# Optimization experiments

Hardware: AMD Instinct MI355X
Metric: run time of the kernel (lower is better)

## Reference

```python
import math
import jax, jax.numpy as jnp
import numpy as np

B, C, NH, H, W = 8, 512, 4, 64, 64
CH = C // 8          # qkv channels = 64
HC = CH // NH        # head channels = 16


def _pos_encoding(c, h, w):
    # Faithful to torch code, including the raw memory reinterpretation of
    # pos_h (h, c) -> (1, c, h, 1) and pos_w (c//2, 2w) -> (1, c, 1, w).
    ph = jnp.arange(h, dtype=jnp.float32)[:, None]            # (h, 1)
    pw = jnp.arange(w, dtype=jnp.float32)[None, :]            # (1, w)
    div = jnp.exp(jnp.arange(0, c, 2, dtype=jnp.float32) * (-(math.log(10000.0) / c)))
    pos_h = ph * div[None, :]                                  # (h, c/2)
    pos_w = pw * div[:, None]                                  # (c/2, w)
    pos_h = jnp.concatenate([jnp.sin(pos_h), jnp.cos(pos_h)], axis=1)  # (h, c)
    pos_w = jnp.concatenate([jnp.sin(pos_w), jnp.cos(pos_w)], axis=1)  # (c/2, 2w)
    pos_h = pos_h.reshape(1, c, h, 1)   # raw view, as in torch
    pos_w = pos_w.reshape(1, c, 1, w)   # raw view, as in torch
    return pos_h + pos_w                # (1, c, h, w)


def _conv1x1(x, w, b):
    return jnp.einsum('bchw,oc->bohw', x, w) + b[None, :, None, None]


def setup_inputs() -> dict:
    key = jax.random.key(0)
    ks = jax.random.split(key, 6)
    s = 0.02
    return {
        'x':  jax.random.normal(ks[0], (B, C, H, W), dtype=jnp.float32),
        'wq': jax.random.normal(ks[1], (CH, C), dtype=jnp.float32) * s,
        'bq': jnp.zeros((CH,), dtype=jnp.float32),
        'wk': jax.random.normal(ks[2], (CH, C), dtype=jnp.float32) * s,
        'bk': jnp.zeros((CH,), dtype=jnp.float32),
        'wv': jax.random.normal(ks[3], (CH, C), dtype=jnp.float32) * s,
        'bv': jnp.zeros((CH,), dtype=jnp.float32),
        'wo': jax.random.normal(ks[4], (C, CH), dtype=jnp.float32) * s,
        'bo': jnp.zeros((C,), dtype=jnp.float32),
        'gamma': jnp.full((1,), 0.5, dtype=jnp.float32),  # nonzero to exercise whole graph
    }


def reference(x, wq, bq, wk, bk, wv, bv, wo, bo, gamma):
    b, c, h, w = x.shape
    nh, hc = NH, HC
    x = x + _pos_encoding(c, h, w)

    q = _conv1x1(x, wq, bq).reshape(b, nh, hc, h, w)
    k = _conv1x1(x, wk, bk).reshape(b, nh, hc, h, w)
    v = _conv1x1(x, wv, bv).reshape(b, nh, hc, h, w)

    # column (H) and row (W) views
    q_H = q.transpose(0, 1, 4, 2, 3).reshape(b * nh * w, hc, h).transpose(0, 2, 1)  # (bnw, h, hc)
    q_W = q.transpose(0, 1, 3, 2, 4).reshape(b * nh * h, hc, w).transpose(0, 2, 1)  # (bnh, w, hc)
    k_H = k.transpose(0, 1, 4, 2, 3).reshape(b * nh * w, hc, h)
    k_W = k.transpose(0, 1, 3, 2, 4).reshape(b * nh * h, hc, w)
    v_H = v.transpose(0, 1, 4, 2, 3).reshape(b * nh * w, hc, h)
    v_W = v.transpose(0, 1, 3, 2, 4).reshape(b * nh * h, hc, w)

    inf_mask = jnp.where(jnp.eye(h, dtype=bool), -jnp.inf, 0.0).astype(x.dtype)  # (h, h)
    energy_H = (jnp.matmul(q_H, k_H) + inf_mask[None]).reshape(b, nh, w, h, h).transpose(0, 2, 1, 3, 4)  # (b,w,nh,h,h)
    energy_W = jnp.matmul(q_W, k_W).reshape(b, nh, h, w, w).transpose(0, 2, 1, 3, 4)                     # (b,h,nh,w,w)

    conc = jax.nn.softmax(jnp.concatenate([energy_H, energy_W], axis=4), axis=4)  # (b,w,nh,h,h+w)

    att_H = conc[..., :h].transpose(0, 2, 1, 3, 4).reshape(b * nh * w, h, h)
    # NOTE: faithful to torch: (b,h,nh,w,w) is flattened in (b,h,nh) order
    att_W = conc[..., h:h + w].reshape(b * nh * h, w, w)

    out_H = jnp.matmul(v_H, att_H.transpose(0, 2, 1))
    out_H = out_H.reshape(b, nh, w, hc, h).transpose(0, 3, 4, 1, 2).reshape(b, nh * hc, h, w)
    out_W = jnp.matmul(v_W, att_W.transpose(0, 2, 1))
    out_W = out_W.reshape(b, nh, h, hc, w).transpose(0, 3, 1, 4, 2).reshape(b, nh * hc, h, w)

    out = _conv1x1(out_H + out_W, wo, bo)
    return gamma * out + x
```

## Files before the change

kernel.cpp:

```cpp
#include <hip/hip_runtime.h>
#include <math.h>


typedef unsigned int u32;
typedef unsigned short u16;
typedef __attribute__((ext_vector_type(8))) short short8;
typedef __attribute__((ext_vector_type(4))) float f32x4;

__device__ __forceinline__ u16 f2bf(float v) {
    u32 u = __float_as_uint(v);
    u32 r = (u + 0x7FFFu + ((u >> 16) & 1u)) >> 16;
    return (u16)r;
}

__device__ __forceinline__ float bf2f(u16 v) {
    return __uint_as_float(((u32)v) << 16);
}

__device__ __forceinline__ void gll16(const void* g, void* l) {
    __builtin_amdgcn_global_load_lds(
        (const __attribute__((address_space(1))) u32*)g,
        (__attribute__((address_space(3))) u32*)l, 16, 0, 0);
}

__global__ __launch_bounds__(64) void pos_kernel(float* __restrict__ PH,
                                                 float* __restrict__ PW) {
    const float r = 0.03597789207798663f;
    int c = blockIdx.x;
    int t = threadIdx.x;
    int i = c >> 3;
    int j = ((c & 7) << 6) | t;
    float ph;
    if (j < 256) ph = sinf((float)i * expf(-(float)j * r));
    else         ph = cosf((float)i * expf(-(float)(j - 256) * r));
    PH[c * 64 + t] = ph;
    int tt = c >> 1;
    float dv = expf(-(float)tt * r);
    PW[c * 64 + t] = (c & 1) ? cosf((float)t * dv) : sinf((float)t * dv);
}

__global__ __launch_bounds__(256) void wconv_kernel(
    const float* __restrict__ wq, const float* __restrict__ wk,
    const float* __restrict__ wv, const float* __restrict__ wo,
    u16* __restrict__ WT, u16* __restrict__ WOb) {
    int i = blockIdx.x * 256 + threadIdx.x;
    if (i < 98304) {
        float v;
        if (i < 32768)      v = wq[i];
        else if (i < 65536) v = wk[i - 32768];
        else                v = wv[i - 65536];
        WT[i] = f2bf(v);
    } else {
        WOb[i - 98304] = f2bf(wo[i - 98304]);
    }
}

__global__ __launch_bounds__(256) void xpose_kernel(
    const float* __restrict__ x, const float* __restrict__ PH,
    const float* __restrict__ PW, u16* __restrict__ XT) {
    __shared__ u16 T[64 * 68];
    int ct = blockIdx.x;
    int pt = blockIdx.y;
    int b  = blockIdx.z;
    int tid = threadIdx.x;
    int c0 = ct * 64;
    const size_t xb = ((size_t)b * 512 + c0) * 4096 + pt * 64;
#pragma unroll
    for (int it = 0; it < 16; ++it) {
        int idx = tid + it * 256;
        int cl = idx >> 6, pl = idx & 63;
        float v = x[xb + (size_t)cl * 4096 + pl]
                + PH[(c0 + cl) * 64 + pt] + PW[(c0 + cl) * 64 + pl];
        T[pl * 68 + cl] = f2bf(v);
    }
    __syncthreads();
#pragma unroll
    for (int jt = 0; jt < 4; ++jt) {
        int row = jt * 16 + (tid >> 4);
        int cq  = tid & 15;
        ushort4 val = *(const ushort4*)&T[row * 68 + cq * 4];
        *(ushort4*)&XT[((size_t)b * 4096 + pt * 64 + row) * 512 + c0 + cq * 4] = val;
    }
}

__global__ __launch_bounds__(256) void qkvm_kernel(
    const u16* __restrict__ XT, const u16* __restrict__ WT,
    const float* __restrict__ bq, const float* __restrict__ bk,
    const float* __restrict__ bv,
    u16* __restrict__ QHt, u16* __restrict__ QWt,
    u16* __restrict__ KHt, u16* __restrict__ KWt,
    u16* __restrict__ VHt, u16* __restrict__ Vb) {
    __shared__ u16 Ab[64 * 64];
    __shared__ u16 Bb[128 * 64];
    int pt = blockIdx.x;
    int mg = blockIdx.y;
    int b  = blockIdx.z;
    int tid  = threadIdx.x;
    int w    = tid >> 6;
    int lane = tid & 63;
    int ln15 = lane & 15, quad = lane >> 4;
    int p0 = pt * 128;
    const u16* Wg = WT + mg * 64 * 512;
    const u16* Xg = XT + ((size_t)b * 4096 + p0) * 512;

    f32x4 acc[4][2];
#pragma unroll
    for (int mf = 0; mf < 4; ++mf)
#pragma unroll
        for (int pf = 0; pf < 2; ++pf)
            acc[mf][pf] = (f32x4){0.f, 0.f, 0.f, 0.f};

    for (int kc = 0; kc < 512; kc += 64) {
        __syncthreads();
#pragma unroll
        for (int it = 0; it < 2; ++it) {
            int idx = tid + it * 256;
            int r = idx >> 3, s = idx & 7;
            gll16(Wg + r * 512 + kc + ((s ^ (r & 7)) * 8), &Ab[idx * 8]);
        }
#pragma unroll
        for (int it = 0; it < 4; ++it) {
            int idx = tid + it * 256;
            int r = idx >> 3, s = idx & 7;
            gll16(Xg + (size_t)r * 512 + kc + ((s ^ (r & 7)) * 8), &Bb[idx * 8]);
        }
        __syncthreads();
#pragma unroll
        for (int ks = 0; ks < 2; ++ks) {
            int cs = ks * 4 + quad;
            short8 af[4], bf[2];
#pragma unroll
            for (int mf = 0; mf < 4; ++mf) {
                int row = mf * 16 + ln15;
                af[mf] = *(const short8*)&Ab[row * 64 + ((cs ^ (row & 7)) * 8)];
            }
#pragma unroll
            for (int pf = 0; pf < 2; ++pf) {
                int row = w * 32 + pf * 16 + ln15;
                bf[pf] = *(const short8*)&Bb[row * 64 + ((cs ^ (row & 7)) * 8)];
            }
#pragma unroll
            for (int mf = 0; mf < 4; ++mf)
#pragma unroll
                for (int pf = 0; pf < 2; ++pf)
                    acc[mf][pf] = __builtin_amdgcn_mfma_f32_16x16x32_bf16(
                        af[mf], bf[pf], acc[mf][pf], 0, 0, 0);
        }
    }

    const float* bias = (mg == 0) ? bq : (mg == 1) ? bk : bv;
    if (mg == 2) {
#pragma unroll
        for (int mf = 0; mf < 4; ++mf)
#pragma unroll
            for (int pf = 0; pf < 2; ++pf) {
                int p = p0 + w * 32 + pf * 16 + ln15;
                int h = p >> 6, wc = p & 63;
#pragma unroll
                for (int reg = 0; reg < 4; ++reg) {
                    int hc = quad * 4 + reg;
                    int m  = mf * 16 + hc;
                    u16 bfv = f2bf(acc[mf][pf][reg] + bias[m]);
                    VHt[(((b * 4 + mf) * 64 + wc) * 16 + hc) * 64 + h] = bfv;
                    Vb[((size_t)(b * 64 + m)) * 4096 + p] = bfv;
                }
            }
    } else {
        u16* Ht = (mg == 1) ? KHt : QHt;
        u16* Wt = (mg == 1) ? KWt : QWt;
#pragma unroll
        for (int mf = 0; mf < 4; ++mf)
#pragma unroll
            for (int pf = 0; pf < 2; ++pf) {
                int p = p0 + w * 32 + pf * 16 + ln15;
                int h = p >> 6, wc = p & 63;
                ushort4 pk;
                pk.x = f2bf(acc[mf][pf][0] + bias[mf * 16 + quad * 4 + 0]);
                pk.y = f2bf(acc[mf][pf][1] + bias[mf * 16 + quad * 4 + 1]);
                pk.z = f2bf(acc[mf][pf][2] + bias[mf * 16 + quad * 4 + 2]);
                pk.w = f2bf(acc[mf][pf][3] + bias[mf * 16 + quad * 4 + 3]);
                *(ushort4*)&Ht[(((b * 4 + mf) * 64 + wc) * 64 + h) * 16 + quad * 4] = pk;
                *(ushort4*)&Wt[(((b * 4 + mf) * 64 + h) * 64 + wc) * 16 + quad * 4] = pk;
            }
    }
}

__global__ __launch_bounds__(256, 4) void attn_kernel(
    const u16* __restrict__ QHt, const u16* __restrict__ QWt,
    const u16* __restrict__ KHt, const u16* __restrict__ KWt,
    const u16* __restrict__ VHt, const u16* __restrict__ Vb,
    u16* __restrict__ OHc, u16* __restrict__ OWc) {
    __shared__ u16 A_lds[64 * 40];
    __shared__ u16 B_lds[128 * 40];
    __shared__ u16 VH_lds[16 * 72];
    __shared__ u16 VW_lds[16 * 72];
    __shared__ u16 P_lds[64 * 152];

    int a = blockIdx.x, n = blockIdx.y, b = blockIdx.z;
    int tid  = threadIdx.x;
    int w    = tid >> 6;
    int lane = tid & 63;
    int ln15 = lane & 15, quad = lane >> 4;
    int nv = a >> 4;
    int hv = ((a & 15) << 2) | n;

    const int cb = ((b * 4 + n) * 64 + a) << 10;
    const u16* vb = Vb + ((size_t)(b * 64 + nv * 16)) * 4096 + hv * 64;

    {
        int t = tid & 127;
        const short8 z8 = {0, 0, 0, 0, 0, 0, 0, 0};
        if (tid < 128) {
            short8 vA = *(const short8*)(QHt + cb + t * 8);
            *(short8*)&A_lds[(t >> 1) * 40 + (t & 1) * 8] = vA;
            short8 vK = *(const short8*)(KHt + cb + t * 8);
            *(short8*)&B_lds[(t >> 1) * 40 + (t & 1) * 8] = vK;
            *(short8*)&B_lds[(t >> 1) * 40 + 16 + (t & 1) * 8] = z8;
            short8 vV = *(const short8*)(VHt + cb + t * 8);
            *(short8*)&VH_lds[(t >> 3) * 72 + (t & 7) * 8] = vV;
        } else {
            short8 vA = *(const short8*)(QWt + cb + t * 8);
            *(short8*)&A_lds[(t >> 1) * 40 + 16 + (t & 1) * 8] = vA;
            short8 vK = *(const short8*)(KWt + cb + t * 8);
            *(short8*)&B_lds[(64 + (t >> 1)) * 40 + 16 + (t & 1) * 8] = vK;
            *(short8*)&B_lds[(64 + (t >> 1)) * 40 + (t & 1) * 8] = z8;
            short8 vV = *(const short8*)(vb + (t >> 3) * 4096 + (t & 7) * 8);
            *(short8*)&VW_lds[(t >> 3) * 72 + (t & 7) * 8] = vV;
        }
    }
    __syncthreads();

    const f32x4 zf = {0.f, 0.f, 0.f, 0.f};
    short8 af = *(const short8*)&A_lds[(w * 16 + ln15) * 40 + quad * 8];
    f32x4 acc[8];
#pragma unroll
    for (int nt = 0; nt < 8; ++nt) {
        short8 bf = *(const short8*)&B_lds[(nt * 16 + ln15) * 40 + quad * 8];
        acc[nt] = __builtin_amdgcn_mfma_f32_16x16x32_bf16(af, bf, zf, 0, 0, 0);
    }

#pragma unroll
    for (int nt = 0; nt < 4; ++nt)
#pragma unroll
        for (int r = 0; r < 4; ++r)
            if (nt * 16 + ln15 == w * 16 + quad * 4 + r) acc[nt][r] = -1e30f;

    float inv[4];
#pragma unroll
    for (int r = 0; r < 4; ++r) {
        float mrow = acc[0][r];
#pragma unroll
        for (int nt = 1; nt < 8; ++nt) mrow = fmaxf(mrow, acc[nt][r]);
        mrow = fmaxf(mrow, __shfl_xor(mrow, 1, 64));
        mrow = fmaxf(mrow, __shfl_xor(mrow, 2, 64));
        mrow = fmaxf(mrow, __shfl_xor(mrow, 4, 64));
        mrow = fmaxf(mrow, __shfl_xor(mrow, 8, 64));
        float s = 0.f;
#pragma unroll
        for (int nt = 0; nt < 8; ++nt) {
            float e = __expf(acc[nt][r] - mrow);
            acc[nt][r] = e;
            s += e;
        }
        s += __shfl_xor(s, 1, 64);
        s += __shfl_xor(s, 2, 64);
        s += __shfl_xor(s, 4, 64);
        s += __shfl_xor(s, 8, 64);
        inv[r] = 1.0f / s;
    }
#pragma unroll
    for (int nt = 0; nt < 8; ++nt)
#pragma unroll
        for (int r = 0; r < 4; ++r)
            P_lds[(w * 16 + quad * 4 + r) * 152 + nt * 16 + ln15] =
                f2bf(acc[nt][r] * inv[r]);
    __syncthreads();

    int prow = (w * 16 + ln15) * 152;
    short8 a0 = *(const short8*)&P_lds[prow +       quad * 8];
    short8 a1 = *(const short8*)&P_lds[prow + 32  + quad * 8];
    short8 a2 = *(const short8*)&P_lds[prow + 64  + quad * 8];
    short8 a3 = *(const short8*)&P_lds[prow + 96  + quad * 8];
    short8 b0 = *(const short8*)&VH_lds[ln15 * 72 +      quad * 8];
    short8 b1 = *(const short8*)&VH_lds[ln15 * 72 + 32 + quad * 8];
    short8 c0 = *(const short8*)&VW_lds[ln15 * 72 +      quad * 8];
    short8 c1 = *(const short8*)&VW_lds[ln15 * 72 + 32 + quad * 8];
    f32x4 oH = __builtin_amdgcn_mfma_f32_16x16x32_bf16(a0, b0, zf, 0, 0, 0);
    oH = __builtin_amdgcn_mfma_f32_16x16x32_bf16(a1, b1, oH, 0, 0, 0);
    f32x4 oW = __builtin_amdgcn_mfma_f32_16x16x32_bf16(a2, c0, zf, 0, 0, 0);
    oW = __builtin_amdgcn_mfma_f32_16x16x32_bf16(a3, c1, oW, 0, 0, 0);

    __syncthreads();
    u16* eph = P_lds;
    u16* epw = P_lds + 16 * 68;
#pragma unroll
    for (int r = 0; r < 4; ++r) {
        eph[(quad * 4 + r) * 68 + ln15 * 4 + w]   = f2bf(oH[r]);
        epw[(w * 16 + quad * 4 + r) * 20 + ln15]  = f2bf(oW[r]);
    }
    __syncthreads();
    {
        int t = tid;
        ushort4 vh = *(const ushort4*)&eph[(t >> 4) * 68 + (t & 15) * 4];
        ushort4 vw = *(const ushort4*)&epw[(t >> 2) * 20 + (t & 3) * 4];
        size_t cbase = (((size_t)b * 4 + n) * 64 + a) * 1024;
        *(ushort4*)&OHc[cbase + t * 4] = vh;
        *(ushort4*)&OWc[cbase + t * 4] = vw;
    }
}

__global__ __launch_bounds__(256) void sconv_kernel(
    const u16* __restrict__ OHc, const u16* __restrict__ OWc,
    u16* __restrict__ Sb) {
    int h = blockIdx.x;
    int b = blockIdx.y;
    int t  = threadIdx.x;
    int wp = t >> 2;
    int cq = t & 3;

    const u16* ohp = OHc + ((((size_t)b * 4 + (h & 3)) * 64 + wp) * 1024
                            + (h >> 2) * 64 + cq * 16);
    short8 oh0 = *(const short8*)ohp;
    short8 oh1 = *(const short8*)(ohp + 8);

    const u16* owb = OWc + (((size_t)b * 4 + (wp & 3)) * 64) * 1024 + h * 16 + cq * 4;
    ushort4 owv[4];
#pragma unroll
    for (int nvi = 0; nvi < 4; ++nvi)
        owv[nvi] = *(const ushort4*)(owb + (size_t)((nvi << 4) | (wp >> 2)) * 1024);

    u16 res[16];
#pragma unroll
    for (int j = 0; j < 16; ++j) {
        u16 ohv = (j < 8) ? (u16)oh0[j] : (u16)oh1[j - 8];
        const ushort4& q = owv[j & 3];
        u16 owu = (j >> 2) == 0 ? q.x : (j >> 2) == 1 ? q.y : (j >> 2) == 2 ? q.z : q.w;
        res[j] = f2bf(bf2f(ohv) + bf2f(owu));
    }
    u16* dst = Sb + (((size_t)b * 4096 + h * 64 + wp) * 64 + cq * 16);
    *(short8*)dst       = *(short8*)&res[0];
    *(short8*)(dst + 8) = *(short8*)&res[8];
}

__global__ __launch_bounds__(256, 4) void finalm_kernel(
    const u16* __restrict__ Sb, const u16* __restrict__ WOb,
    const float* __restrict__ bo, const float* __restrict__ gamma,
    const float* __restrict__ x, const float* __restrict__ PH,
    const float* __restrict__ PW, float* __restrict__ out) {
    __shared__ u16 Ab[64 * 64];
    __shared__ u16 Bb[128 * 64];
    int pt = blockIdx.x;
    int mc = blockIdx.y;
    int b  = blockIdx.z;
    int tid  = threadIdx.x;
    int w    = tid >> 6;
    int lane = tid & 63;
    int ln15 = lane & 15, quad = lane >> 4;
    int p0 = pt * 128, m0 = mc * 64;

    float4 xv[4][2];
#pragma unroll
    for (int mf = 0; mf < 4; ++mf) {
        int m = m0 + mf * 16 + ln15;
#pragma unroll
        for (int pf = 0; pf < 2; ++pf) {
            int pb = p0 + w * 32 + pf * 16 + quad * 4;
            xv[mf][pf] = *(const float4*)&x[((size_t)(b * 512 + m)) * 4096 + pb];
        }
    }

    const u16* Ag = WOb + m0 * 64;
    const u16* Sg = Sb + ((size_t)b * 4096 + p0) * 64;

#pragma unroll
    for (int it = 0; it < 2; ++it) {
        int idx = tid + it * 256;
        int r = idx >> 3, s = idx & 7;
        gll16(Ag + r * 64 + ((s ^ (r & 7)) * 8), &Ab[idx * 8]);
    }
#pragma unroll
    for (int it = 0; it < 4; ++it) {
        int idx = tid + it * 256;
        int r = idx >> 3, s = idx & 7;
        gll16(Sg + r * 64 + ((s ^ (r & 7)) * 8), &Bb[idx * 8]);
    }
    __syncthreads();

    const f32x4 zf = {0.f, 0.f, 0.f, 0.f};
    f32x4 acc[4][2];
#pragma unroll
    for (int mf = 0; mf < 4; ++mf)
#pragma unroll
        for (int pf = 0; pf < 2; ++pf)
            acc[mf][pf] = zf;
#pragma unroll
    for (int ks = 0; ks < 2; ++ks) {
        int cs = ks * 4 + quad;
        short8 af[2], bf[4];
#pragma unroll
        for (int pf = 0; pf < 2; ++pf) {
            int row = w * 32 + pf * 16 + ln15;
            af[pf] = *(const short8*)&Bb[row * 64 + ((cs ^ (row & 7)) * 8)];
        }
#pragma unroll
        for (int mf = 0; mf < 4; ++mf) {
            int row = mf * 16 + ln15;
            bf[mf] = *(const short8*)&Ab[row * 64 + ((cs ^ (row & 7)) * 8)];
        }
#pragma unroll
        for (int mf = 0; mf < 4; ++mf)
#pragma unroll
            for (int pf = 0; pf < 2; ++pf)
                acc[mf][pf] = __builtin_amdgcn_mfma_f32_16x16x32_bf16(
                    af[pf], bf[mf], acc[mf][pf], 0, 0, 0);
    }

    float g = gamma[0];
    int h = pt * 2 + (w >> 1);
    int plb = (w & 1) * 32;
#pragma unroll
    for (int mf = 0; mf < 4; ++mf) {
        int m = m0 + mf * 16 + ln15;
        float bm = bo[m];
        float ph = PH[m * 64 + h];
#pragma unroll
        for (int pf = 0; pf < 2; ++pf) {
            int pb = p0 + w * 32 + pf * 16 + quad * 4;
            size_t o = ((size_t)(b * 512 + m)) * 4096 + pb;
            float4 pwv = *(const float4*)&PW[m * 64 + plb + pf * 16 + quad * 4];
            float4 res;
            res.x = g * (acc[mf][pf][0] + bm) + xv[mf][pf].x + ph + pwv.x;
            res.y = g * (acc[mf][pf][1] + bm) + xv[mf][pf].y + ph + pwv.y;
            res.z = g * (acc[mf][pf][2] + bm) + xv[mf][pf].z + ph + pwv.z;
            res.w = g * (acc[mf][pf][3] + bm) + xv[mf][pf].w + ph + pwv.w;
            *(float4*)&out[o] = res;
        }
    }
}

extern "C" void kernel_launch(void* const* d_in, const int* in_sizes, int n_in,
                              void* d_out, int out_size, void* d_ws, size_t ws_size,
                              hipStream_t stream) {
    const float* x     = (const float*)d_in[0];
    const float* wq    = (const float*)d_in[1];
    const float* bq    = (const float*)d_in[2];
    const float* wk    = (const float*)d_in[3];
    const float* bk    = (const float*)d_in[4];
    const float* wv    = (const float*)d_in[5];
    const float* bv    = (const float*)d_in[6];
    const float* wo    = (const float*)d_in[7];
    const float* bo    = (const float*)d_in[8];
    const float* gamma = (const float*)d_in[9];
    float* out = (float*)d_out;
    float* ws  = (float*)d_ws;

    float* PH = ws;
    float* PW = PH + 32768;
    u16*   WT  = (u16*)(PW + 32768);
    u16*   WOb = WT + 98304;
    u16*   XT  = WOb + 32768;
    u16*   QHt = XT + 16777216;
    u16*   QWt = QHt + 2097152;
    u16*   KHt = QWt + 2097152;
    u16*   KWt = KHt + 2097152;
    u16*   VHt = KWt + 2097152;
    u16*   Vb  = VHt + 2097152;
    u16*   OHc = XT;
    u16*   OWc = OHc + 2097152;
    u16*   Sbb = OWc + 2097152;

    pos_kernel<<<dim3(512), dim3(64), 0, stream>>>(PH, PW);
    wconv_kernel<<<dim3(512), dim3(256), 0, stream>>>(wq, wk, wv, wo, WT, WOb);
    xpose_kernel<<<dim3(8, 64, 8), dim3(256), 0, stream>>>(x, PH, PW, XT);
    qkvm_kernel<<<dim3(32, 3, 8), dim3(256), 0, stream>>>(
        XT, WT, bq, bk, bv, QHt, QWt, KHt, KWt, VHt, Vb);
    attn_kernel<<<dim3(64, 4, 8), dim3(256), 0, stream>>>(
        QHt, QWt, KHt, KWt, VHt, Vb, OHc, OWc);
    sconv_kernel<<<dim3(64, 8), dim3(256), 0, stream>>>(OHc, OWc, Sbb);
    finalm_kernel<<<dim3(32, 8, 8), dim3(256), 0, stream>>>(
        Sbb, WOb, bo, gamma, x, PH, PW, out);
}
```

Measured before the change: 207.7 us.

## Fuse x transpose into QKV GEMM and fold positional encoding into weight projections

Removes the separate transpose kernel that wrote a bf16 copy of x plus positional encoding. The QKV kernel now reads fp32 x directly, converts it to bf16 in LDS, and computes all 192 output channels per block, so each x tile is loaded once. The positional-encoding contribution is precomputed as W·PH and W·PW tables by a small kernel and added in the epilogue, using linearity of the 1x1 conv. The attention kernel also packs its LDS buffers into one shared union with smaller strides to raise occupancy, which needs an extra barrier before P is written. The risks are uncoalesced-ish strided x loads and the positional term being added in fp32 rather than quantised with x.

```diff
diff --git a/kernel.cpp b/kernel.cpp
--- a/kernel.cpp
+++ b/kernel.cpp
@@ -55,133 +55,117 @@
     }
 }
 
-__global__ __launch_bounds__(256) void xpose_kernel(
-    const float* __restrict__ x, const float* __restrict__ PH,
-    const float* __restrict__ PW, u16* __restrict__ XT) {
-    __shared__ u16 T[64 * 68];
-    int ct = blockIdx.x;
-    int pt = blockIdx.y;
-    int b  = blockIdx.z;
-    int tid = threadIdx.x;
-    int c0 = ct * 64;
-    const size_t xb = ((size_t)b * 512 + c0) * 4096 + pt * 64;
-#pragma unroll
-    for (int it = 0; it < 16; ++it) {
-        int idx = tid + it * 256;
-        int cl = idx >> 6, pl = idx & 63;
-        float v = x[xb + (size_t)cl * 4096 + pl]
-                + PH[(c0 + cl) * 64 + pt] + PW[(c0 + cl) * 64 + pl];
-        T[pl * 68 + cl] = f2bf(v);
-    }
-    __syncthreads();
-#pragma unroll
-    for (int jt = 0; jt < 4; ++jt) {
-        int row = jt * 16 + (tid >> 4);
-        int cq  = tid & 15;
-        ushort4 val = *(const ushort4*)&T[row * 68 + cq * 4];
-        *(ushort4*)&XT[((size_t)b * 4096 + pt * 64 + row) * 512 + c0 + cq * 4] = val;
-    }
-}
-
-__global__ __launch_bounds__(256) void qkvm_kernel(
-    const u16* __restrict__ XT, const u16* __restrict__ WT,
+__global__ __launch_bounds__(256) void wpos_kernel(
+    const float* __restrict__ wq, const float* __restrict__ wk,
+    const float* __restrict__ wv,
+    const float* __restrict__ PH, const float* __restrict__ PW,
+    float* __restrict__ WPH3, float* __restrict__ WPW3) {
+    int gid = blockIdx.x * 256 + threadIdx.x;
+    int h = gid & 63;
+    int m = (gid >> 6) & 63;
+    int t = gid >> 12;
+    int mg = t >> 1, tbl = t & 1;
+    const float* W = (mg == 0) ? wq : (mg == 1) ? wk : wv;
+    const float* P = tbl ? PW : PH;
+    const float* wr = W + m * 512;
+    float s = 0.f;
+#pragma unroll 8
+    for (int c = 0; c < 512; ++c) s += wr[c] * P[c * 64 + h];
+    (tbl ? WPW3 : WPH3)[(mg * 64 + m) * 64 + h] = s;
+}
+
+__global__ __launch_bounds__(256) void qkvx_kernel(
+    const float* __restrict__ x, const u16* __restrict__ WT,
     const float* __restrict__ bq, const float* __restrict__ bk,
     const float* __restrict__ bv,
+    const float* __restrict__ WPH3, const float* __restrict__ WPW3,
     u16* __restrict__ QHt, u16* __restrict__ QWt,
     u16* __restrict__ KHt, u16* __restrict__ KWt,
     u16* __restrict__ VHt, u16* __restrict__ Vb) {
-    __shared__ u16 Ab[64 * 64];
-    __shared__ u16 Bb[128 * 64];
-    int pt = blockIdx.x;
-    int mg = blockIdx.y;
-    int b  = blockIdx.z;
+    __shared__ u16 Wb[192 * 64];
+    __shared__ u16 Bb[64 * 64];
+    int L  = blockIdx.x;
+    int b  = L & 7;
+    int pt = L >> 3;
     int tid  = threadIdx.x;
     int w    = tid >> 6;
     int lane = tid & 63;
     int ln15 = lane & 15, quad = lane >> 4;
-    int p0 = pt * 128;
-    const u16* Wg = WT + mg * 64 * 512;
-    const u16* Xg = XT + ((size_t)b * 4096 + p0) * 512;
-
-    f32x4 acc[4][2];
-#pragma unroll
-    for (int mf = 0; mf < 4; ++mf)
-#pragma unroll
-        for (int pf = 0; pf < 2; ++pf)
-            acc[mf][pf] = (f32x4){0.f, 0.f, 0.f, 0.f};
+
+    f32x4 acc[12];
+#pragma unroll
+    for (int mf = 0; mf < 12; ++mf) acc[mf] = (f32x4){0.f, 0.f, 0.f, 0.f};
+
+    const float* xb = x + (size_t)b * 2097152 + pt * 64;
 
     for (int kc = 0; kc < 512; kc += 64) {
         __syncthreads();
 #pragma unroll
-        for (int it = 0; it < 2; ++it) {
+        for (int it = 0; it < 6; ++it) {
             int idx = tid + it * 256;
             int r = idx >> 3, s = idx & 7;
-            gll16(Wg + r * 512 + kc + ((s ^ (r & 7)) * 8), &Ab[idx * 8]);
-        }
-#pragma unroll
-        for (int it = 0; it < 4; ++it) {
-            int idx = tid + it * 256;
-            int r = idx >> 3, s = idx & 7;
-            gll16(Xg + (size_t)r * 512 + kc + ((s ^ (r & 7)) * 8), &Bb[idx * 8]);
+            gll16(WT + r * 512 + kc + ((s ^ (r & 7)) * 8), &Wb[idx * 8]);
+        }
+#pragma unroll
+        for (int j = 0; j < 2; ++j) {
+            int cc = w + j * 4;
+            const float* xp = xb + (size_t)(kc + cc * 8) * 4096 + lane;
+            float v[8];
+#pragma unroll
+            for (int i = 0; i < 8; ++i) v[i] = xp[(size_t)i * 4096];
+            short8 pk;
+#pragma unroll
+            for (int i = 0; i < 8; ++i) pk[i] = (short)f2bf(v[i]);
+            *(short8*)&Bb[lane * 64 + ((cc ^ (lane & 7)) * 8)] = pk;
         }
         __syncthreads();
 #pragma unroll
         for (int ks = 0; ks < 2; ++ks) {
             int cs = ks * 4 + quad;
-            short8 af[4], bf[2];
-#pragma unroll
-            for (int mf = 0; mf < 4; ++mf) {
-                int row = mf * 16 + ln15;
-                af[mf] = *(const short8*)&Ab[row * 64 + ((cs ^ (row & 7)) * 8)];
+            int brow = w * 16 + ln15;
+            short8 bf = *(const short8*)&Bb[brow * 64 + ((cs ^ (brow & 7)) * 8)];
+#pragma unroll
+            for (int mf = 0; mf < 12; ++mf) {
+                int arow = mf * 16 + ln15;
+                short8 af = *(const short8*)&Wb[arow * 64 + ((cs ^ (arow & 7)) * 8)];
+                acc[mf] = __builtin_amdgcn_mfma_f32_16x16x32_bf16(
+                    af, bf, acc[mf], 0, 0, 0);
             }
-#pragma unroll
-            for (int pf = 0; pf < 2; ++pf) {
-                int row = w * 32 + pf * 16 + ln15;
-                bf[pf] = *(const short8*)&Bb[row * 64 + ((cs ^ (row & 7)) * 8)];
+        }
+    }
+
+    int wc = w * 16 + ln15;
+#pragma unroll
+    for (int mf = 0; mf < 12; ++mf) {
+        int mg = mf >> 2, nm = mf & 3;
+        const float* bias = (mg == 0) ? bq : (mg == 1) ? bk : bv;
+        float vals[4];
+#pragma unroll
+        for (int reg = 0; reg < 4; ++reg) {
+            int m2 = nm * 16 + quad * 4 + reg;
+            vals[reg] = acc[mf][reg] + bias[m2]
+                      + WPH3[(mg * 64 + m2) * 64 + pt]
+                      + WPW3[(mg * 64 + m2) * 64 + wc];
+        }
+        if (mg == 2) {
+#pragma unroll
+            for (int reg = 0; reg < 4; ++reg) {
+                int hc = quad * 4 + reg;
+                u16 bv16 = f2bf(vals[reg]);
+                VHt[(((b * 4 + nm) * 64 + wc) * 16 + hc) * 64 + pt] = bv16;
+                Vb[((size_t)(b * 64 + nm * 16 + hc)) * 4096 + pt * 64 + wc] = bv16;
             }
-#pragma unroll
-            for (int mf = 0; mf < 4; ++mf)
-#pragma unroll
-                for (int pf = 0; pf < 2; ++pf)
-                    acc[mf][pf] = __builtin_amdgcn_mfma_f32_16x16x32_bf16(
-                        af[mf], bf[pf], acc[mf][pf], 0, 0, 0);
-        }
-    }
-
-    const float* bias = (mg == 0) ? bq : (mg == 1) ? bk : bv;
-    if (mg == 2) {
-#pragma unroll
-        for (int mf = 0; mf < 4; ++mf)
-#pragma unroll
-            for (int pf = 0; pf < 2; ++pf) {
-                int p = p0 + w * 32 + pf * 16 + ln15;
-                int h = p >> 6, wc = p & 63;
-#pragma unroll
-                for (int reg = 0; reg < 4; ++reg) {
-                    int hc = quad * 4 + reg;
-                    int m  = mf * 16 + hc;
-                    u16 bfv = f2bf(acc[mf][pf][reg] + bias[m]);
-                    VHt[(((b * 4 + mf) * 64 + wc) * 16 + hc) * 64 + h] = bfv;
-                    Vb[((size_t)(b * 64 + m)) * 4096 + p] = bfv;
-                }
-            }
-    } else {
-        u16* Ht = (mg == 1) ? KHt : QHt;
-        u16* Wt = (mg == 1) ? KWt : QWt;
-#pragma unroll
-        for (int mf = 0; mf < 4; ++mf)
-#pragma unroll
-            for (int pf = 0; pf < 2; ++pf) {
-                int p = p0 + w * 32 + pf * 16 + ln15;
-                int h = p >> 6, wc = p & 63;
-                ushort4 pk;
-                pk.x = f2bf(acc[mf][pf][0] + bias[mf * 16 + quad * 4 + 0]);
-                pk.y = f2bf(acc[mf][pf][1] + bias[mf * 16 + quad * 4 + 1]);
-                pk.z = f2bf(acc[mf][pf][2] + bias[mf * 16 + quad * 4 + 2]);
-                pk.w = f2bf(acc[mf][pf][3] + bias[mf * 16 + quad * 4 + 3]);
-                *(ushort4*)&Ht[(((b * 4 + mf) * 64 + wc) * 64 + h) * 16 + quad * 4] = pk;
-                *(ushort4*)&Wt[(((b * 4 + mf) * 64 + h) * 64 + wc) * 16 + quad * 4] = pk;
-            }
+        } else {
+            u16* Ht = (mg == 1) ? KHt : QHt;
+            u16* Wt = (mg == 1) ? KWt : QWt;
+            ushort4 pk;
+            pk.x = f2bf(vals[0]);
+            pk.y = f2bf(vals[1]);
+            pk.z = f2bf(vals[2]);
+            pk.w = f2bf(vals[3]);
+            *(ushort4*)&Ht[(((b * 4 + nm) * 64 + wc) * 64 + pt) * 16 + quad * 4] = pk;
+            *(ushort4*)&Wt[(((b * 4 + nm) * 64 + pt) * 64 + wc) * 16 + quad * 4] = pk;
+        }
     }
 }
 
@@ -190,11 +174,12 @@
     const u16* __restrict__ KHt, const u16* __restrict__ KWt,
     const u16* __restrict__ VHt, const u16* __restrict__ Vb,
     u16* __restrict__ OHc, u16* __restrict__ OWc) {
-    __shared__ u16 A_lds[64 * 40];
-    __shared__ u16 B_lds[128 * 40];
-    __shared__ u16 VH_lds[16 * 72];
-    __shared__ u16 VW_lds[16 * 72];
-    __shared__ u16 P_lds[64 * 152];
+    __shared__ u16 U[11008];
+    u16* A_lds  = U;
+    u16* B_lds  = U + 2560;
+    u16* P_lds  = U;
+    u16* VH_lds = U + 8704;
+    u16* VW_lds = U + 9856;
 
     int a = blockIdx.x, n = blockIdx.y, b = blockIdx.z;
     int tid  = threadIdx.x;
@@ -214,16 +199,16 @@
             short8 vA = *(const short8*)(QHt + cb + t * 8);
             *(short8*)&A_lds[(t >> 1) * 40 + (t & 1) * 8] = vA;
             short8 vK = *(const short8*)(KHt + cb + t * 8);
-            *(short8*)&B_lds[(t >> 1) * 40 + (t & 1) * 8] = vK;
-            *(short8*)&B_lds[(t >> 1) * 40 + 16 + (t & 1) * 8] = z8;
+            *(short8*)&B_lds[(t >> 1) * 48 + (t & 1) * 8] = vK;
+            *(short8*)&B_lds[(t >> 1) * 48 + 16 + (t & 1) * 8] = z8;
             short8 vV = *(const short8*)(VHt + cb + t * 8);
             *(short8*)&VH_lds[(t >> 3) * 72 + (t & 7) * 8] = vV;
         } else {
             short8 vA = *(const short8*)(QWt + cb + t * 8);
             *(short8*)&A_lds[(t >> 1) * 40 + 16 + (t & 1) * 8] = vA;
             short8 vK = *(const short8*)(KWt + cb + t * 8);
-            *(short8*)&B_lds[(64 + (t >> 1)) * 40 + 16 + (t & 1) * 8] = vK;
-            *(short8*)&B_lds[(64 + (t >> 1)) * 40 + (t & 1) * 8] = z8;
+            *(short8*)&B_lds[(64 + (t >> 1)) * 48 + 16 + (t & 1) * 8] = vK;
+            *(short8*)&B_lds[(64 + (t >> 1)) * 48 + (t & 1) * 8] = z8;
             short8 vV = *(const short8*)(vb + (t >> 3) * 4096 + (t & 7) * 8);
             *(short8*)&VW_lds[(t >> 3) * 72 + (t & 7) * 8] = vV;
         }
@@ -235,7 +220,7 @@
     f32x4 acc[8];
 #pragma unroll
     for (int nt = 0; nt < 8; ++nt) {
-        short8 bf = *(const short8*)&B_lds[(nt * 16 + ln15) * 40 + quad * 8];
+        short8 bf = *(const short8*)&B_lds[(nt * 16 + ln15) * 48 + quad * 8];
         acc[nt] = __builtin_amdgcn_mfma_f32_16x16x32_bf16(af, bf, zf, 0, 0, 0);
     }
 
@@ -268,15 +253,16 @@
         s += __shfl_xor(s, 8, 64);
         inv[r] = 1.0f / s;
     }
+    __syncthreads();
 #pragma unroll
     for (int nt = 0; nt < 8; ++nt)
 #pragma unroll
         for (int r = 0; r < 4; ++r)
-            P_lds[(w * 16 + quad * 4 + r) * 152 + nt * 16 + ln15] =
+            P_lds[(w * 16 + quad * 4 + r) * 136 + nt * 16 + ln15] =
                 f2bf(acc[nt][r] * inv[r]);
     __syncthreads();
 
-    int prow = (w * 16 + ln15) * 152;
+    int prow = (w * 16 + ln15) * 136;
     short8 a0 = *(const short8*)&P_lds[prow +       quad * 8];
     short8 a1 = *(const short8*)&P_lds[prow + 32  + quad * 8];
     short8 a2 = *(const short8*)&P_lds[prow + 64  + quad * 8];
@@ -291,8 +277,8 @@
     oW = __builtin_amdgcn_mfma_f32_16x16x32_bf16(a3, c1, oW, 0, 0, 0);
 
     __syncthreads();
-    u16* eph = P_lds;
-    u16* epw = P_lds + 16 * 68;
+    u16* eph = U;
+    u16* epw = U + 16 * 68;
 #pragma unroll
     for (int r = 0; r < 4; ++r) {
         eph[(quad * 4 + r) * 68 + ln15 * 4 + w]   = f2bf(oH[r]);
@@ -454,26 +440,27 @@
     float* out = (float*)d_out;
     float* ws  = (float*)d_ws;
 
-    float* PH = ws;
-    float* PW = PH + 32768;
-    u16*   WT  = (u16*)(PW + 32768);
-    u16*   WOb = WT + 98304;
-    u16*   XT  = WOb + 32768;
-    u16*   QHt = XT + 16777216;
-    u16*   QWt = QHt + 2097152;
-    u16*   KHt = QWt + 2097152;
-    u16*   KWt = KHt + 2097152;
-    u16*   VHt = KWt + 2097152;
-    u16*   Vb  = VHt + 2097152;
-    u16*   OHc = XT;
-    u16*   OWc = OHc + 2097152;
-    u16*   Sbb = OWc + 2097152;
+    float* PH   = ws;
+    float* PW   = PH + 32768;
+    float* WPH3 = PW + 32768;
+    float* WPW3 = WPH3 + 12288;
+    u16*   WT   = (u16*)(WPW3 + 12288);
+    u16*   WOb  = WT + 98304;
+    u16*   QHt  = WOb + 32768;
+    u16*   QWt  = QHt + 2097152;
+    u16*   KHt  = QWt + 2097152;
+    u16*   KWt  = KHt + 2097152;
+    u16*   VHt  = KWt + 2097152;
+    u16*   Vb   = VHt + 2097152;
+    u16*   OHc  = Vb  + 2097152;
+    u16*   OWc  = OHc + 2097152;
+    u16*   Sbb  = OWc + 2097152;
 
     pos_kernel<<<dim3(512), dim3(64), 0, stream>>>(PH, PW);
     wconv_kernel<<<dim3(512), dim3(256), 0, stream>>>(wq, wk, wv, wo, WT, WOb);
-    xpose_kernel<<<dim3(8, 64, 8), dim3(256), 0, stream>>>(x, PH, PW, XT);
-    qkvm_kernel<<<dim3(32, 3, 8), dim3(256), 0, stream>>>(
-        XT, WT, bq, bk, bv, QHt, QWt, KHt, KWt, VHt, Vb);
+    wpos_kernel<<<dim3(96), dim3(256), 0, stream>>>(wq, wk, wv, PH, PW, WPH3, WPW3);
+    qkvx_kernel<<<dim3(512), dim3(256), 0, stream>>>(
+        x, WT, bq, bk, bv, WPH3, WPW3, QHt, QWt, KHt, KWt, VHt, Vb);
     attn_kernel<<<dim3(64, 4, 8), dim3(256), 0, stream>>>(
         QHt, QWt, KHt, KWt, VHt, Vb, OHc, OWc);
     sconv_kernel<<<dim3(64, 8), dim3(256), 0, stream>>>(OHc, OWc, Sbb);
```

New measurement: 207.3 us. No clear change (-0.2%).
